# Performance work log

Measured on AMD Instinct MI355X. Metric: run time of the kernel, lower is better.

## Reference

```python
import jax, jax.numpy as jnp
import numpy as np

D_MODEL = 1024
NUM_HEADS = 16
DEPTH = D_MODEL // NUM_HEADS
B, S = 2, 2048


def setup_inputs() -> dict:
    key = jax.random.key(0)
    ks = jax.random.split(key, 12)
    scale = 1.0 / np.sqrt(D_MODEL)
    inp = {
        "q": jax.random.normal(ks[0], (B, S, D_MODEL), dtype=jnp.float32),
        "k": jax.random.normal(ks[1], (B, S, D_MODEL), dtype=jnp.float32),
        "v": jax.random.normal(ks[2], (B, S, D_MODEL), dtype=jnp.float32),
        "mask": jax.random.uniform(ks[3], (B, 1, S, S), dtype=jnp.float32),
        # Linear params, torch convention: y = x @ W.T + b
        "Wq": jax.random.normal(ks[4], (D_MODEL, D_MODEL), dtype=jnp.float32) * scale,
        "bq": jnp.zeros((D_MODEL,), dtype=jnp.float32),
        "Wk": jax.random.normal(ks[5], (D_MODEL, D_MODEL), dtype=jnp.float32) * scale,
        "bk": jnp.zeros((D_MODEL,), dtype=jnp.float32),
        "Wv": jax.random.normal(ks[6], (D_MODEL, D_MODEL), dtype=jnp.float32) * scale,
        "bv": jnp.zeros((D_MODEL,), dtype=jnp.float32),
        "Wo": jax.random.normal(ks[7], (D_MODEL, D_MODEL), dtype=jnp.float32) * scale,
        "bo": jnp.zeros((D_MODEL,), dtype=jnp.float32),
    }
    return inp


def _split_heads(x):
    # [B, S, D] -> [B, H, S, depth]
    b, s, _ = x.shape
    return x.reshape(b, s, NUM_HEADS, DEPTH).transpose(0, 2, 1, 3)


def reference(q, k, v, mask, Wq, bq, Wk, bk, Wv, bv, Wo, bo):
    qh = _split_heads(q @ Wq.T + bq)
    kh = _split_heads(k @ Wk.T + bk)
    vh = _split_heads(v @ Wv.T + bv)
    # scaled dot-product attention, full [B,H,S,S] scores (as in source)
    logits = jnp.einsum("bhqd,bhkd->bhqk", qh, kh) / jnp.sqrt(
        jnp.asarray(DEPTH, dtype=jnp.float32)
    )
    logits = logits + mask * 1e-09  # faithful to source (mask * 1e-9)
    weights = jax.nn.softmax(logits, axis=-1)
    attn = jnp.einsum("bhqk,bhkd->bhqd", weights, vh)
    attn = attn.transpose(0, 2, 1, 3).reshape(q.shape[0], -1, D_MODEL)
    out = attn @ Wo.T + bo
    return (out, weights)
```

## Files before the change

kernel.cpp:

```cpp
#include <hip/hip_runtime.h>


typedef _Float16 half8 __attribute__((ext_vector_type(8)));
typedef float    floatx4 __attribute__((ext_vector_type(4)));

#define MFMA16(a, b, c) __builtin_amdgcn_mfma_f32_16x16x32_f16((a), (b), (c), 0, 0, 0)

#define D_MODEL 1024
#define S_LEN   2048
#define NHEAD   16
#define DEPTH   64
#define BATCH   2

__device__ __forceinline__ void gld_lds16(const _Float16* g, _Float16* l) {
    __builtin_amdgcn_global_load_lds(
        (const __attribute__((address_space(1))) unsigned int*)g,
        (__attribute__((address_space(3))) unsigned int*)l, 16, 0, 0);
}

__global__ void cvt_kernel(const float* __restrict__ src, _Float16* __restrict__ dst, int n8) {
    int i = blockIdx.x * 256 + threadIdx.x;
    if (i < n8) {
        const floatx4* s = (const floatx4*)src + (size_t)i * 2;
        floatx4 f0 = s[0], f1 = s[1];
        half8 h;
#pragma unroll
        for (int j = 0; j < 4; ++j) { h[j] = (_Float16)f0[j]; h[4 + j] = (_Float16)f1[j]; }
        *((half8*)dst + i) = h;
    }
}

template <int MODE>
__global__ __launch_bounds__(256) void gemm_kernel(
    const _Float16* __restrict__ X, const _Float16* __restrict__ W,
    const float* __restrict__ bias, void* __restrict__ outp)
{
    __shared__ _Float16 A_lds[128 * 32];
    __shared__ _Float16 B_lds[128 * 32];

    const int tid  = threadIdx.x;
    const int lane = tid & 63;
    const int w    = tid >> 6;
    const int r15  = lane & 15;
    const int quad = lane >> 4;
    const int wr   = w >> 1, wc = w & 1;
    const int bn   = blockIdx.x;
    const int bm   = blockIdx.y;

    const int srow = w * 16 + (lane >> 2);
    const int sseg = lane & 3;
    const _Float16* ag = X + (size_t)(bm * 128 + srow) * 1024 + sseg * 8;
    const _Float16* bg = W + (size_t)(bn * 128 + srow) * 1024 + sseg * 8;
    _Float16* al = &A_lds[srow * 32 + sseg * 8];
    _Float16* bl = &B_lds[srow * 32 + sseg * 8];

    floatx4 acc[4][4];
#pragma unroll
    for (int t = 0; t < 4; ++t)
#pragma unroll
        for (int u = 0; u < 4; ++u) acc[t][u] = floatx4{0.f, 0.f, 0.f, 0.f};

    for (int k0 = 0; k0 < 1024; k0 += 32) {
        __syncthreads();
        gld_lds16(ag + k0, al);
        gld_lds16(ag + k0 + (size_t)64 * 1024, al + 64 * 32);
        gld_lds16(bg + k0, bl);
        gld_lds16(bg + k0 + (size_t)64 * 1024, bl + 64 * 32);
        __syncthreads();
        half8 a[4], bf[4];
#pragma unroll
        for (int t = 0; t < 4; ++t)
            a[t] = *(const half8*)&A_lds[(wr * 64 + t * 16 + r15) * 32 + quad * 8];
#pragma unroll
        for (int u = 0; u < 4; ++u)
            bf[u] = *(const half8*)&B_lds[(wc * 64 + u * 16 + r15) * 32 + quad * 8];
#pragma unroll
        for (int t = 0; t < 4; ++t)
#pragma unroll
            for (int u = 0; u < 4; ++u) acc[t][u] = MFMA16(a[t], bf[u], acc[t][u]);
    }

    const int gc0 = bn * 128 + wc * 64;
    float bb[4];
#pragma unroll
    for (int u = 0; u < 4; ++u) bb[u] = bias[gc0 + u * 16 + r15];

#pragma unroll
    for (int t = 0; t < 4; ++t) {
#pragma unroll
        for (int u = 0; u < 4; ++u) {
            const int gc = gc0 + u * 16 + r15;
#pragma unroll
            for (int r = 0; r < 4; ++r) {
                const int grow = bm * 128 + wr * 64 + t * 16 + quad * 4 + r;
                const float val = acc[t][u][r] + bb[u];
                if constexpr (MODE == 0) {
                    const int hh = gc >> 6, dd = gc & 63;
                    const int b_ = grow >> 11, s = grow & 2047;
                    ((_Float16*)outp)[((size_t)((b_ * 16 + hh) * 2048 + s)) * 64 + dd] =
                        (_Float16)val;
                } else if constexpr (MODE == 2) {
                    const int hh = gc >> 6, dd = gc & 63;
                    const int b_ = grow >> 11, s = grow & 2047;
                    ((_Float16*)outp)[((size_t)((b_ * 16 + hh) * 64 + dd)) * 2048 + s] =
                        (_Float16)val;
                } else {
                    ((float*)outp)[(size_t)grow * 1024 + gc] = val;
                }
            }
        }
    }
}

__global__ __launch_bounds__(256, 2) void attn_kernel(
    const _Float16* __restrict__ Q, const _Float16* __restrict__ K,
    const _Float16* __restrict__ Vt, float* __restrict__ wout,
    _Float16* __restrict__ attn_out)
{
    __shared__ _Float16 w_lds[16 * 1032];
    __shared__ float red[2][4][16];

    const int tid  = threadIdx.x;
    const int lane = tid & 63;
    const int wv   = tid >> 6;
    const int r15  = lane & 15;
    const int quad = lane >> 4;
    const int qb   = blockIdx.x;
    const int h    = blockIdx.y;
    const int b    = blockIdx.z;

    const size_t hoff = ((size_t)(b * 16 + h)) * S_LEN * DEPTH;
    const _Float16* Qh  = Q + hoff + (size_t)qb * 16 * DEPTH;
    const _Float16* Kh  = K + hoff;
    const _Float16* Vth = Vt + hoff;

    half8 q0 = *(const half8*)(Qh + r15 * 64 + quad * 8);
    half8 q1 = *(const half8*)(Qh + r15 * 64 + 32 + quad * 8);

    floatx4 S[32];
#pragma unroll
    for (int kt = 0; kt < 32; ++kt) {
        const _Float16* kp = Kh + (size_t)(kt * 64 + wv * 16 + r15) * 64 + quad * 8;
        half8 b0 = *(const half8*)kp;
        half8 b1 = *(const half8*)(kp + 32);
        floatx4 z = floatx4{0.f, 0.f, 0.f, 0.f};
        z = MFMA16(q0, b0, z);
        z = MFMA16(q1, b1, z);
        S[kt] = z;
    }

    float pm[4] = {-1e30f, -1e30f, -1e30f, -1e30f};
#pragma unroll
    for (int kt = 0; kt < 32; ++kt)
#pragma unroll
        for (int j = 0; j < 4; ++j) {
            S[kt][j] *= 0.125f;
            pm[j] = fmaxf(pm[j], S[kt][j]);
        }
#pragma unroll
    for (int m = 1; m <= 8; m <<= 1)
#pragma unroll
        for (int j = 0; j < 4; ++j) pm[j] = fmaxf(pm[j], __shfl_xor(pm[j], m, 64));
#pragma unroll
    for (int j = 0; j < 4; ++j)
        if (r15 == j) red[0][wv][quad * 4 + j] = pm[j];
    __syncthreads();
    float gm[4];
#pragma unroll
    for (int j = 0; j < 4; ++j) {
        int row = quad * 4 + j;
        gm[j] = fmaxf(fmaxf(red[0][0][row], red[0][1][row]),
                      fmaxf(red[0][2][row], red[0][3][row]));
    }
    float ps[4] = {0.f, 0.f, 0.f, 0.f};
#pragma unroll
    for (int kt = 0; kt < 32; ++kt)
#pragma unroll
        for (int j = 0; j < 4; ++j) {
            float e = __expf(S[kt][j] - gm[j]);
            S[kt][j] = e;
            ps[j] += e;
        }
#pragma unroll
    for (int m = 1; m <= 8; m <<= 1)
#pragma unroll
        for (int j = 0; j < 4; ++j) ps[j] += __shfl_xor(ps[j], m, 64);
#pragma unroll
    for (int j = 0; j < 4; ++j)
        if (r15 == j) red[1][wv][quad * 4 + j] = ps[j];
    __syncthreads();
    float gl[4];
#pragma unroll
    for (int j = 0; j < 4; ++j) {
        int row = quad * 4 + j;
        gl[j] = 1.0f / (red[1][0][row] + red[1][1][row] + red[1][2][row] + red[1][3][row]);
    }

    float* wrow = wout + (((size_t)(b * 16 + h)) * S_LEN + (size_t)qb * 16) * S_LEN;
    floatx4 oacc = floatx4{0.f, 0.f, 0.f, 0.f};
#pragma unroll
    for (int hf = 0; hf < 2; ++hf) {
#pragma unroll
        for (int k2 = 0; k2 < 16; ++k2) {
            const int kt = hf * 16 + k2;
#pragma unroll
            for (int j = 0; j < 4; ++j)
                w_lds[(quad * 4 + j) * 1032 + k2 * 64 + wv * 16 + r15] =
                    (_Float16)(S[kt][j] * gl[j]);
        }
        __syncthreads();
#pragma unroll
        for (int k2 = 0; k2 < 16; ++k2) {
            const int kt = hf * 16 + k2;
#pragma unroll
            for (int j = 0; j < 4; ++j)
                wrow[(size_t)(quad * 4 + j) * 2048 + kt * 64 + wv * 16 + r15] =
                    S[kt][j] * gl[j];
            const _Float16* vp =
                Vth + (size_t)(wv * 16 + r15) * 2048 + (size_t)kt * 64 + quad * 8;
            half8 a0 = *(const half8*)&w_lds[r15 * 1032 + k2 * 64 + quad * 8];
            half8 a1 = *(const half8*)&w_lds[r15 * 1032 + k2 * 64 + 32 + quad * 8];
            half8 b0 = *(const half8*)vp;
            half8 b1 = *(const half8*)(vp + 32);
            oacc = MFMA16(a0, b0, oacc);
            oacc = MFMA16(a1, b1, oacc);
        }
        __syncthreads();
    }

    _Float16* ao = attn_out + ((size_t)(b * S_LEN + qb * 16)) * D_MODEL + h * 64 + wv * 16;
#pragma unroll
    for (int r = 0; r < 4; ++r)
        ao[(size_t)(quad * 4 + r) * D_MODEL + r15] = (_Float16)oacc[r];
}

extern "C" void kernel_launch(void* const* d_in, const int* in_sizes, int n_in,
                              void* d_out, int out_size, void* d_ws, size_t ws_size,
                              hipStream_t stream)
{
    const float* q  = (const float*)d_in[0];
    const float* k  = (const float*)d_in[1];
    const float* v  = (const float*)d_in[2];
    const float* Wq = (const float*)d_in[4];
    const float* bq = (const float*)d_in[5];
    const float* Wk = (const float*)d_in[6];
    const float* bk = (const float*)d_in[7];
    const float* Wv = (const float*)d_in[8];
    const float* bv = (const float*)d_in[9];
    const float* Wo = (const float*)d_in[10];
    const float* bo = (const float*)d_in[11];

    const size_t NTOK = (size_t)BATCH * S_LEN * D_MODEL;
    const size_t WSZ  = (size_t)D_MODEL * D_MODEL;
    _Float16* base = (_Float16*)d_ws;
    _Float16* qh  = base;
    _Float16* kh  = base + NTOK;
    _Float16* vh  = base + 2 * NTOK;
    _Float16* Qw  = base + 3 * NTOK;
    _Float16* Kw  = base + 4 * NTOK;
    _Float16* Vt  = base + 5 * NTOK;
    _Float16* Wqh = base + 6 * NTOK;
    _Float16* Wkh = Wqh + WSZ;
    _Float16* Wvh = Wkh + WSZ;
    _Float16* Woh = Wvh + WSZ;
    _Float16* Aw  = qh;

    float* out  = (float*)d_out;
    float* wout = out + NTOK;

    dim3 blk(256);
    cvt_kernel<<<dim3(2048), blk, 0, stream>>>(q, qh, (int)(NTOK / 8));
    cvt_kernel<<<dim3(2048), blk, 0, stream>>>(k, kh, (int)(NTOK / 8));
    cvt_kernel<<<dim3(2048), blk, 0, stream>>>(v, vh, (int)(NTOK / 8));
    cvt_kernel<<<dim3(512),  blk, 0, stream>>>(Wq, Wqh, (int)(WSZ / 8));
    cvt_kernel<<<dim3(512),  blk, 0, stream>>>(Wk, Wkh, (int)(WSZ / 8));
    cvt_kernel<<<dim3(512),  blk, 0, stream>>>(Wv, Wvh, (int)(WSZ / 8));
    cvt_kernel<<<dim3(512),  blk, 0, stream>>>(Wo, Woh, (int)(WSZ / 8));

    dim3 ggrid(8, 32);
    gemm_kernel<0><<<ggrid, blk, 0, stream>>>(qh, Wqh, bq, (void*)Qw);
    gemm_kernel<0><<<ggrid, blk, 0, stream>>>(kh, Wkh, bk, (void*)Kw);
    gemm_kernel<2><<<ggrid, blk, 0, stream>>>(vh, Wvh, bv, (void*)Vt);

    attn_kernel<<<dim3(128, 16, 2), blk, 0, stream>>>(Qw, Kw, Vt, wout, Aw);

    gemm_kernel<1><<<ggrid, blk, 0, stream>>>(Aw, Woh, bo, (void*)out);
}
```

Measured before the change: 992.1 us.

## Recompute QK scores in attention instead of holding full score rows in registers

The attention kernel no longer keeps all 32 score tiles in registers. A first pass computes the row max and sum with an online-softmax recurrence. A second pass recomputes QK^T per tile, writes the normalized weights with nontemporal stores, and multiplies by V through a small double-buffered LDS tile. This frees registers and LDS so launch bounds can target 4 blocks per CU, and block indices are remapped to group work across heads and batches. The cost is doubled QK MFMA work, K loaded twice, and one barrier per tile.

Measured after the change: 996.3 us. Within noise of the previous version (+0.4%).

```diff
diff --git a/kernel.cpp b/kernel.cpp
--- a/kernel.cpp
+++ b/kernel.cpp
@@ -112,22 +112,26 @@
     }
 }
 
-__global__ __launch_bounds__(256, 2) void attn_kernel(
+__global__ __launch_bounds__(256, 4) void attn_kernel(
     const _Float16* __restrict__ Q, const _Float16* __restrict__ K,
     const _Float16* __restrict__ Vt, float* __restrict__ wout,
     _Float16* __restrict__ attn_out)
 {
-    __shared__ _Float16 w_lds[16 * 1032];
-    __shared__ float red[2][4][16];
+    __shared__ _Float16 w_s[2][16 * 72];
+    __shared__ float red_m[4][16];
+    __shared__ float red_l[4][16];
 
     const int tid  = threadIdx.x;
     const int lane = tid & 63;
     const int wv   = tid >> 6;
     const int r15  = lane & 15;
     const int quad = lane >> 4;
-    const int qb   = blockIdx.x;
-    const int h    = blockIdx.y;
-    const int b    = blockIdx.z;
+
+    const int orig = blockIdx.x + 128 * (blockIdx.y + 16 * blockIdx.z);
+    const int work = (orig & 7) * 512 + (orig >> 3);
+    const int qb = work & 127;
+    const int h  = (work >> 7) & 15;
+    const int b  = work >> 11;
 
     const size_t hoff = ((size_t)(b * 16 + h)) * S_LEN * DEPTH;
     const _Float16* Qh  = Q + hoff + (size_t)qb * 16 * DEPTH;
@@ -137,95 +141,87 @@
     half8 q0 = *(const half8*)(Qh + r15 * 64 + quad * 8);
     half8 q1 = *(const half8*)(Qh + r15 * 64 + 32 + quad * 8);
 
-    floatx4 S[32];
-#pragma unroll
+    const _Float16* kbase = Kh + (size_t)(wv * 16 + r15) * 64 + quad * 8;
+
+    float m[4], l[4];
+#pragma unroll
+    for (int j = 0; j < 4; ++j) { m[j] = -1e30f; l[j] = 0.f; }
+
+#pragma unroll 4
     for (int kt = 0; kt < 32; ++kt) {
-        const _Float16* kp = Kh + (size_t)(kt * 64 + wv * 16 + r15) * 64 + quad * 8;
+        const _Float16* kp = kbase + (size_t)kt * 4096;
         half8 b0 = *(const half8*)kp;
         half8 b1 = *(const half8*)(kp + 32);
         floatx4 z = floatx4{0.f, 0.f, 0.f, 0.f};
         z = MFMA16(q0, b0, z);
         z = MFMA16(q1, b1, z);
-        S[kt] = z;
-    }
-
-    float pm[4] = {-1e30f, -1e30f, -1e30f, -1e30f};
-#pragma unroll
-    for (int kt = 0; kt < 32; ++kt)
 #pragma unroll
         for (int j = 0; j < 4; ++j) {
-            S[kt][j] *= 0.125f;
-            pm[j] = fmaxf(pm[j], S[kt][j]);
-        }
-#pragma unroll
-    for (int m = 1; m <= 8; m <<= 1)
-#pragma unroll
-        for (int j = 0; j < 4; ++j) pm[j] = fmaxf(pm[j], __shfl_xor(pm[j], m, 64));
+            float s  = z[j] * 0.125f;
+            float nm = fmaxf(m[j], s);
+            l[j] = l[j] * __expf(m[j] - nm) + __expf(s - nm);
+            m[j] = nm;
+        }
+    }
+#pragma unroll
+    for (int mk = 1; mk <= 8; mk <<= 1)
+#pragma unroll
+        for (int j = 0; j < 4; ++j) {
+            float om = __shfl_xor(m[j], mk, 64);
+            float ol = __shfl_xor(l[j], mk, 64);
+            float nm = fmaxf(m[j], om);
+            l[j] = l[j] * __expf(m[j] - nm) + ol * __expf(om - nm);
+            m[j] = nm;
+        }
 #pragma unroll
     for (int j = 0; j < 4; ++j)
-        if (r15 == j) red[0][wv][quad * 4 + j] = pm[j];
+        if (r15 == j) { red_m[wv][quad * 4 + j] = m[j]; red_l[wv][quad * 4 + j] = l[j]; }
     __syncthreads();
-    float gm[4];
+    float gm[4], gli[4];
 #pragma unroll
     for (int j = 0; j < 4; ++j) {
-        int row = quad * 4 + j;
-        gm[j] = fmaxf(fmaxf(red[0][0][row], red[0][1][row]),
-                      fmaxf(red[0][2][row], red[0][3][row]));
-    }
-    float ps[4] = {0.f, 0.f, 0.f, 0.f};
-#pragma unroll
-    for (int kt = 0; kt < 32; ++kt)
+        const int row = quad * 4 + j;
+        float m0 = red_m[0][row], m1 = red_m[1][row];
+        float m2 = red_m[2][row], m3 = red_m[3][row];
+        float mm = fmaxf(fmaxf(m0, m1), fmaxf(m2, m3));
+        float ll = red_l[0][row] * __expf(m0 - mm) + red_l[1][row] * __expf(m1 - mm)
+                 + red_l[2][row] * __expf(m2 - mm) + red_l[3][row] * __expf(m3 - mm);
+        gm[j]  = mm;
+        gli[j] = 1.0f / ll;
+    }
+
+    float* wrow = wout + (((size_t)(b * 16 + h)) * S_LEN + (size_t)qb * 16) * S_LEN;
+    const _Float16* vbase = Vth + (size_t)(wv * 16 + r15) * 2048 + quad * 8;
+    floatx4 oacc = floatx4{0.f, 0.f, 0.f, 0.f};
+
+    for (int kt = 0; kt < 32; ++kt) {
+        const _Float16* kp = kbase + (size_t)kt * 4096;
+        half8 kb0 = *(const half8*)kp;
+        half8 kb1 = *(const half8*)(kp + 32);
+        const _Float16* vp = vbase + (size_t)kt * 64;
+        half8 vb0 = *(const half8*)vp;
+        half8 vb1 = *(const half8*)(vp + 32);
+
+        floatx4 z = floatx4{0.f, 0.f, 0.f, 0.f};
+        z = MFMA16(q0, kb0, z);
+        z = MFMA16(q1, kb1, z);
+
+        _Float16* ws = &w_s[kt & 1][0];
 #pragma unroll
         for (int j = 0; j < 4; ++j) {
-            float e = __expf(S[kt][j] - gm[j]);
-            S[kt][j] = e;
-            ps[j] += e;
-        }
-#pragma unroll
-    for (int m = 1; m <= 8; m <<= 1)
-#pragma unroll
-        for (int j = 0; j < 4; ++j) ps[j] += __shfl_xor(ps[j], m, 64);
-#pragma unroll
-    for (int j = 0; j < 4; ++j)
-        if (r15 == j) red[1][wv][quad * 4 + j] = ps[j];
-    __syncthreads();
-    float gl[4];
-#pragma unroll
-    for (int j = 0; j < 4; ++j) {
-        int row = quad * 4 + j;
-        gl[j] = 1.0f / (red[1][0][row] + red[1][1][row] + red[1][2][row] + red[1][3][row]);
-    }
-
-    float* wrow = wout + (((size_t)(b * 16 + h)) * S_LEN + (size_t)qb * 16) * S_LEN;
-    floatx4 oacc = floatx4{0.f, 0.f, 0.f, 0.f};
-#pragma unroll
-    for (int hf = 0; hf < 2; ++hf) {
-#pragma unroll
-        for (int k2 = 0; k2 < 16; ++k2) {
-            const int kt = hf * 16 + k2;
-#pragma unroll
-            for (int j = 0; j < 4; ++j)
-                w_lds[(quad * 4 + j) * 1032 + k2 * 64 + wv * 16 + r15] =
-                    (_Float16)(S[kt][j] * gl[j]);
-        }
-        __syncthreads();
-#pragma unroll
-        for (int k2 = 0; k2 < 16; ++k2) {
-            const int kt = hf * 16 + k2;
-#pragma unroll
-            for (int j = 0; j < 4; ++j)
-                wrow[(size_t)(quad * 4 + j) * 2048 + kt * 64 + wv * 16 + r15] =
-                    S[kt][j] * gl[j];
-            const _Float16* vp =
-                Vth + (size_t)(wv * 16 + r15) * 2048 + (size_t)kt * 64 + quad * 8;
-            half8 a0 = *(const half8*)&w_lds[r15 * 1032 + k2 * 64 + quad * 8];
-            half8 a1 = *(const half8*)&w_lds[r15 * 1032 + k2 * 64 + 32 + quad * 8];
-            half8 b0 = *(const half8*)vp;
-            half8 b1 = *(const half8*)(vp + 32);
-            oacc = MFMA16(a0, b0, oacc);
-            oacc = MFMA16(a1, b1, oacc);
-        }
-        __syncthreads();
+            float e = __expf(z[j] * 0.125f - gm[j]) * gli[j];
+            ws[(quad * 4 + j) * 72 + wv * 16 + r15] = (_Float16)e;
+            __builtin_nontemporal_store(
+                e, &wrow[(size_t)(quad * 4 + j) * 2048 + kt * 64 + wv * 16 + r15]);
+        }
+        asm volatile("s_waitcnt lgkmcnt(0)" ::: "memory");
+        __builtin_amdgcn_s_barrier();
+        __builtin_amdgcn_sched_barrier(0);
+
+        half8 a0 = *(const half8*)&ws[r15 * 72 + quad * 8];
+        half8 a1 = *(const half8*)&ws[r15 * 72 + 32 + quad * 8];
+        oacc = MFMA16(a0, vb0, oacc);
+        oacc = MFMA16(a1, vb1, oacc);
     }
 
     _Float16* ao = attn_out + ((size_t)(b * S_LEN + qb * 16)) * D_MODEL + h * 64 + wv * 16;
```
